# Performance work log

Hardware: AMD Instinct MI355X
Metric: run time of the kernel (lower is better)

## Reference

```python
import jax, jax.numpy as jnp
import numpy as np

NUM_CLASSES = 6
POOL = 'avg'


def setup_inputs() -> dict:
    key = jax.random.key(0)
    k1, k2, k3, k4 = jax.random.split(key, 4)
    B, T, C, Hf, Wf = 16, 24, 128, 32, 32
    H, W = 128, 128
    out_temporal = jax.random.normal(k1, (B, T, C, Hf, Wf), dtype=jnp.float32)
    gt = jax.random.randint(k2, (B, T, H, W), 0, NUM_CLASSES, dtype=jnp.int64)
    positions = jnp.sort(jax.random.randint(k3, (B, T), 0, 365, dtype=jnp.int64), axis=-1)
    sits_id = jax.random.randint(k4, (B,), 0, 10000, dtype=jnp.int64)
    return {'out_temporal': out_temporal, 'gt': gt, 'positions': positions, 'sits_id': sits_id}


def compute_majority(gt, num_classes):
    # gt: [B,T,H,W] int -> [B,T] majority class per (b,t)
    # batched bincount: one-hot count over flattened pixels, then argmax
    B, T = gt.shape[0], gt.shape[1]
    gt_flat = gt.reshape(B, T, -1)                                   # [B,T,HW]
    classes = jnp.arange(num_classes, dtype=gt.dtype)                # [K]
    counts = (gt_flat[..., None] == classes).sum(axis=2, dtype=jnp.int32)  # [B,T,K]
    return jnp.argmax(counts, axis=-1).astype(jnp.int64)             # first-max tie-break, matches torch


def reference(out_temporal, gt, positions, sits_id):
    # spatial pooling of temporal encoder output: [B,T,C,Hf,Wf] -> [B,T,C]
    if POOL == 'avg':
        emb = out_temporal.mean(axis=(-2, -1))
    else:
        emb = out_temporal.max(axis=(-2, -1))
    emb = emb[:, :, None, :]                       # [B,T,1,C]  (P=1)
    labels = compute_majority(gt, NUM_CLASSES)     # [B,T]
    labels = labels[:, :, None]                    # [B,T,1]
    return emb, labels, sits_id, positions
```

## Files before the change

### kernel.cpp

```cpp
#include <hip/hip_runtime.h>
#include <hip/hip_bf16.h>


#define NCHAN     49152
#define SPATIAL   1024
#define NBT       384
#define PIX_PER_BT 16384
#define NUM_CLASSES 6

#define OFF_EMB   0
#define OFF_LAB   49152
#define OFF_SITS  49536
#define OFF_POS   49552

__global__ void mean_pool_kernel(const float* __restrict__ in,
                                 float* __restrict__ out) {
    const int lane  = threadIdx.x & 63;
    const int wave  = (blockIdx.x * blockDim.x + threadIdx.x) >> 6;
    const int nwave = (gridDim.x * blockDim.x) >> 6;
    for (int c = wave; c < NCHAN; c += nwave) {
        const float4* p = (const float4*)(in + (size_t)c * SPATIAL);
        float s = 0.0f;
#pragma unroll
        for (int i = 0; i < 4; ++i) {
            float4 v = p[lane + 64 * i];
            s += (v.x + v.y) + (v.z + v.w);
        }
#pragma unroll
        for (int off = 32; off > 0; off >>= 1)
            s += __shfl_down(s, off, 64);
        if (lane == 0)
            out[OFF_EMB + c] = s * (1.0f / (float)SPATIAL);
    }
}

__global__ void majority_kernel(const int* __restrict__ gt,
                                const int* __restrict__ positions,
                                const int* __restrict__ sits_id,
                                float* __restrict__ out) {
    const int bt = blockIdx.x;
    const int4* p4 = (const int4*)(gt + (size_t)bt * PIX_PER_BT);

    int cnt[NUM_CLASSES] = {0, 0, 0, 0, 0, 0};
    for (int i = threadIdx.x; i < PIX_PER_BT / 4; i += 256) {
        int4 v = p4[i];
#pragma unroll
        for (int c = 0; c < NUM_CLASSES; ++c) {
            cnt[c] += (v.x == c) + (v.y == c) + (v.z == c) + (v.w == c);
        }
    }

    __shared__ int scnt[NUM_CLASSES];
    if (threadIdx.x < NUM_CLASSES) scnt[threadIdx.x] = 0;
    __syncthreads();

#pragma unroll
    for (int c = 0; c < NUM_CLASSES; ++c) {
        int s = cnt[c];
#pragma unroll
        for (int off = 32; off > 0; off >>= 1)
            s += __shfl_down(s, off, 64);
        if ((threadIdx.x & 63) == 0) atomicAdd(&scnt[c], s);
    }
    __syncthreads();

    if (threadIdx.x == 0) {
        int best = 0, bc = scnt[0];
#pragma unroll
        for (int c = 1; c < NUM_CLASSES; ++c) {
            if (scnt[c] > bc) { bc = scnt[c]; best = c; }
        }
        out[OFF_LAB + bt] = (float)best;
        out[OFF_POS + bt] = (float)positions[bt];
        if (bt < 16) out[OFF_SITS + bt] = (float)sits_id[bt];
    }
}

extern "C" void kernel_launch(void* const* d_in, const int* in_sizes, int n_in,
                              void* d_out, int out_size, void* d_ws, size_t ws_size,
                              hipStream_t stream) {
    const float* out_temporal = (const float*)d_in[0];
    const int*   gt           = (const int*)d_in[1];
    const int*   positions    = (const int*)d_in[2];
    const int*   sits_id      = (const int*)d_in[3];
    float*       out          = (float*)d_out;

    mean_pool_kernel<<<2048, 256, 0, stream>>>(out_temporal, out);

    majority_kernel<<<NBT, 256, 0, stream>>>(gt, positions, sits_id, out);
}
```

Baseline: 296.3 us.

## Fuse mean-pool and majority kernels into one launch with more loads in flight

Merges the spatial mean-pool and majority-label kernels into one 1024-thread kernel whose blocks are split by index between the two jobs. Each mean-pool wave now issues all loads for four channels up front and writes the four results as one float4. Each majority block loads its whole pixel slice in four int4 loads per thread with no loop. The aim is to remove one launch, let both memory-bound phases run at the same time, and raise memory-level parallelism. The cost is higher register use per thread and coarse 1024-thread blocks, which may limit occupancy.

Result: no change. 292.1 us (-1.4%).

```diff
diff --git a/kernel.cpp b/kernel.cpp
--- a/kernel.cpp
+++ b/kernel.cpp
@@ -2,10 +2,10 @@
 #include <hip/hip_bf16.h>
 
 
-#define NCHAN     49152
-#define SPATIAL   1024
-#define NBT       384
-#define PIX_PER_BT 16384
+#define NCHAN       49152
+#define SPATIAL     1024
+#define NBT         384
+#define PIX_PER_BT  16384
 #define NUM_CLASSES 6
 
 #define OFF_EMB   0
@@ -13,66 +13,99 @@
 #define OFF_SITS  49536
 #define OFF_POS   49552
 
-__global__ void mean_pool_kernel(const float* __restrict__ in,
-                                 float* __restrict__ out) {
-    const int lane  = threadIdx.x & 63;
-    const int wave  = (blockIdx.x * blockDim.x + threadIdx.x) >> 6;
-    const int nwave = (gridDim.x * blockDim.x) >> 6;
-    for (int c = wave; c < NCHAN; c += nwave) {
-        const float4* p = (const float4*)(in + (size_t)c * SPATIAL);
-        float s = 0.0f;
+#define MEAN_BLOCKS 768
+#define TOTAL_BLOCKS (MEAN_BLOCKS + NBT)
+
+__global__ __launch_bounds__(1024) void fused_kernel(
+        const float* __restrict__ in,
+        const int*  __restrict__ gt,
+        const int*  __restrict__ positions,
+        const int*  __restrict__ sits_id,
+        float* __restrict__ out) {
+    const int tid  = threadIdx.x;
+    const int lane = tid & 63;
+    const int wave = tid >> 6;
+
+    if (blockIdx.x < MEAN_BLOCKS) {
+        const int c0 = blockIdx.x * 64 + wave * 4;
+        const float4* p0 = (const float4*)(in + (size_t)(c0 + 0) * SPATIAL);
+        const float4* p1 = (const float4*)(in + (size_t)(c0 + 1) * SPATIAL);
+        const float4* p2 = (const float4*)(in + (size_t)(c0 + 2) * SPATIAL);
+        const float4* p3 = (const float4*)(in + (size_t)(c0 + 3) * SPATIAL);
+
+        float4 v0[4], v1[4], v2[4], v3[4];
+#pragma unroll
+        for (int i = 0; i < 4; ++i) v0[i] = p0[lane + 64 * i];
+#pragma unroll
+        for (int i = 0; i < 4; ++i) v1[i] = p1[lane + 64 * i];
+#pragma unroll
+        for (int i = 0; i < 4; ++i) v2[i] = p2[lane + 64 * i];
+#pragma unroll
+        for (int i = 0; i < 4; ++i) v3[i] = p3[lane + 64 * i];
+
+        float s0 = 0.f, s1 = 0.f, s2 = 0.f, s3 = 0.f;
 #pragma unroll
         for (int i = 0; i < 4; ++i) {
-            float4 v = p[lane + 64 * i];
-            s += (v.x + v.y) + (v.z + v.w);
+            s0 += (v0[i].x + v0[i].y) + (v0[i].z + v0[i].w);
+            s1 += (v1[i].x + v1[i].y) + (v1[i].z + v1[i].w);
+            s2 += (v2[i].x + v2[i].y) + (v2[i].z + v2[i].w);
+            s3 += (v3[i].x + v3[i].y) + (v3[i].z + v3[i].w);
         }
+
 #pragma unroll
-        for (int off = 32; off > 0; off >>= 1)
-            s += __shfl_down(s, off, 64);
-        if (lane == 0)
-            out[OFF_EMB + c] = s * (1.0f / (float)SPATIAL);
-    }
-}
+        for (int off = 32; off > 0; off >>= 1) {
+            s0 += __shfl_down(s0, off, 64);
+            s1 += __shfl_down(s1, off, 64);
+            s2 += __shfl_down(s2, off, 64);
+            s3 += __shfl_down(s3, off, 64);
+        }
+        if (lane == 0) {
+            const float k = 1.0f / (float)SPATIAL;
+            float4 r = make_float4(s0 * k, s1 * k, s2 * k, s3 * k);
+            *(float4*)(out + OFF_EMB + c0) = r;
+        }
+    } else {
+        const int bt = blockIdx.x - MEAN_BLOCKS;
+        const int4* p4 = (const int4*)(gt + (size_t)bt * PIX_PER_BT);
 
-__global__ void majority_kernel(const int* __restrict__ gt,
-                                const int* __restrict__ positions,
-                                const int* __restrict__ sits_id,
-                                float* __restrict__ out) {
-    const int bt = blockIdx.x;
-    const int4* p4 = (const int4*)(gt + (size_t)bt * PIX_PER_BT);
+        int4 w0 = p4[tid + 1024 * 0];
+        int4 w1 = p4[tid + 1024 * 1];
+        int4 w2 = p4[tid + 1024 * 2];
+        int4 w3 = p4[tid + 1024 * 3];
 
-    int cnt[NUM_CLASSES] = {0, 0, 0, 0, 0, 0};
-    for (int i = threadIdx.x; i < PIX_PER_BT / 4; i += 256) {
-        int4 v = p4[i];
+        int cnt[NUM_CLASSES];
 #pragma unroll
         for (int c = 0; c < NUM_CLASSES; ++c) {
-            cnt[c] += (v.x == c) + (v.y == c) + (v.z == c) + (v.w == c);
+            cnt[c] = (w0.x == c) + (w0.y == c) + (w0.z == c) + (w0.w == c)
+                   + (w1.x == c) + (w1.y == c) + (w1.z == c) + (w1.w == c)
+                   + (w2.x == c) + (w2.y == c) + (w2.z == c) + (w2.w == c)
+                   + (w3.x == c) + (w3.y == c) + (w3.z == c) + (w3.w == c);
         }
-    }
 
-    __shared__ int scnt[NUM_CLASSES];
-    if (threadIdx.x < NUM_CLASSES) scnt[threadIdx.x] = 0;
-    __syncthreads();
+        __shared__ int scnt[NUM_CLASSES];
+        if (tid < NUM_CLASSES) scnt[tid] = 0;
+        __syncthreads();
 
 #pragma unroll
-    for (int c = 0; c < NUM_CLASSES; ++c) {
-        int s = cnt[c];
+        for (int c = 0; c < NUM_CLASSES; ++c) {
+            int s = cnt[c];
 #pragma unroll
-        for (int off = 32; off > 0; off >>= 1)
-            s += __shfl_down(s, off, 64);
-        if ((threadIdx.x & 63) == 0) atomicAdd(&scnt[c], s);
-    }
-    __syncthreads();
+            for (int off = 32; off > 0; off >>= 1)
+                s += __shfl_down(s, off, 64);
+            if (lane == 0) atomicAdd(&scnt[c], s);
+        }
+        __syncthreads();
 
-    if (threadIdx.x == 0) {
-        int best = 0, bc = scnt[0];
+        if (tid == 0) {
+            int best = 0, bc = scnt[0];
 #pragma unroll
-        for (int c = 1; c < NUM_CLASSES; ++c) {
-            if (scnt[c] > bc) { bc = scnt[c]; best = c; }
+            for (int c = 1; c < NUM_CLASSES; ++c) {
+                if (scnt[c] > bc) { bc = scnt[c]; best = c; }
+            }
+            out[OFF_LAB + bt] = (float)best;
+            out[OFF_POS + bt] = (float)positions[bt];
+            if (bt < 16) out[OFF_SITS + bt] = (float)sits_id[bt];
         }
-        out[OFF_LAB + bt] = (float)best;
-        out[OFF_POS + bt] = (float)positions[bt];
-        if (bt < 16) out[OFF_SITS + bt] = (float)sits_id[bt];
     }
 }
 
@@ -85,7 +118,5 @@
     const int*   sits_id      = (const int*)d_in[3];
     float*       out          = (float*)d_out;
 
-    mean_pool_kernel<<<2048, 256, 0, stream>>>(out_temporal, out);
-
-    majority_kernel<<<NBT, 256, 0, stream>>>(gt, positions, sits_id, out);
+    fused_kernel<<<TOTAL_BLOCKS, 1024, 0, stream>>>(out_temporal, gt, positions, sits_id, out);
 }
```
